# Performance work log

Hardware: AMD Instinct MI355X
Metric: run time of the kernel (lower is better)

## Reference

```python
import jax, jax.numpy as jnp
import numpy as np
import math

MUL = 16                      # num_in_features == num_out_features
LDIMS = (1, 3, 5)             # 0e, 1o, 2e  (lmax = 2)
FEAT = MUL * sum(LDIMS)       # 144 = irreps dim = number_of_basis
PATHS = [(0,0,0),(1,1,0),(2,2,0),
         (0,1,1),(1,0,1),(1,2,1),(2,1,1),
         (0,2,2),(1,1,2),(2,0,2),(2,2,2)]
DOT_PATHS = [(0,0,0),(1,1,0),(2,2,0)]

# ---------- real Wigner-3j / Clebsch-Gordan (e3nn convention), numpy precompute ----------

def _su2_cg(j1, m1, j2, m2, j3, m3):
    if m3 != m1 + m2:
        return 0.0
    f = math.factorial
    vmin = max(-j1 + j2 + m3, -j1 + m1, 0)
    vmax = min(j2 + j3 + m1, j3 - j1 + j2, j3 + m3)
    C = math.sqrt((2*j3+1) * f(j3+j1-j2) * f(j3-j1+j2) * f(j1+j2-j3)
                  * f(j3+m3) * f(j3-m3)
                  / (f(j1+j2+j3+1) * f(j1-m1) * f(j1+m1) * f(j2-m2) * f(j2+m2)))
    S = 0.0
    for v in range(vmin, vmax + 1):
        S += (-1.0)**(v + j2 + m2) * f(j2+j3+m1-v) * f(j1-m1+v) / (
            f(v) * f(j3-j1+j2-v) * f(j3+m3-v) * f(v+j1-j2-m3))
    return C * S

def _qmat(l):
    # complex -> real spherical-harmonic change of basis (e3nn convention)
    q = np.zeros((2*l+1, 2*l+1), dtype=np.complex128)
    for m in range(-l, 0):
        q[l+m, l+abs(m)] = 1.0/math.sqrt(2)
        q[l+m, l-abs(m)] = -1j/math.sqrt(2)
    q[l, l] = 1.0
    for m in range(1, l+1):
        q[l+m, l+abs(m)] = (-1)**m/math.sqrt(2)
        q[l+m, l-abs(m)] = 1j*(-1)**m/math.sqrt(2)
    return (-1j)**l * q

def _real_w3j(l1, l2, l3):
    C = np.zeros((2*l1+1, 2*l2+1, 2*l3+1))
    for i, m1 in enumerate(range(-l1, l1+1)):
        for j, m2 in enumerate(range(-l2, l2+1)):
            for k, m3 in enumerate(range(-l3, l3+1)):
                C[i, j, k] = _su2_cg(l1, m1, l2, m2, l3, m3)
    Cr = np.einsum('ij,kl,mn,ikn->jlm', _qmat(l1), _qmat(l2),
                   np.conj(_qmat(l3).T), C.astype(np.complex128))
    Cr = np.real(Cr)
    return (Cr / np.linalg.norm(Cr)).astype(np.float32)  # unit Frobenius norm (3j convention)

W3J = {p: _real_w3j(*p) for p in set(PATHS)}

# ---------- fully connected tensor product (component/element normalization) ----------

def _split(x):
    # blocked layout: [mul x 0e | mul x 1o | mul x 2e]
    n = x.shape[0]
    xs, o = [], 0
    for d in LDIMS:
        xs.append(x[:, o:o + MUL*d].reshape(n, MUL, d))
        o += MUL * d
    return xs

def _fctp(x1, x2, W):
    # W: [11, u, v, w] stacked per PATHS
    xs1, xs2 = _split(x1), _split(x2)
    n = x1.shape[0]
    n_paths = {l3: sum(1 for p in PATHS if p[2] == l3) for l3 in range(3)}
    outs = [None, None, None]
    for i, (l1, l2, l3) in enumerate(PATHS):
        C = jnp.asarray(W3J[(l1, l2, l3)])          # [i, j, k]
        scale = math.sqrt((2*l3 + 1) / (n_paths[l3] * MUL * MUL))
        a = jnp.einsum('nvj,ijk->nivk', xs2[l2], C)      # [n, i, v, k]
        b = jnp.einsum('nui,nivk->nuvk', xs1[l1], a)     # [n, u, v, k]
        o = scale * jnp.einsum('nuvk,uvw->nwk', b, W[i]) # [n, w, k]
        outs[l3] = o if outs[l3] is None else outs[l3] + o
    return jnp.concatenate([o.reshape(n, -1) for o in outs], axis=1)  # [n, 9*MUL]

def _dot(x1, x2, Wd):
    # FCTP(irreps_input, irreps_input, '0e'): paths (0,0,0),(1,1,0),(2,2,0), out mul = 1
    xs1, xs2 = _split(x1), _split(x2)
    fan = 3 * MUL * MUL
    acc = 0.0
    for i, (l1, l2, l3) in enumerate(DOT_PATHS):
        C = jnp.asarray(W3J[(l1, l2, l3)])[:, :, 0]      # [i, j]
        t = jnp.einsum('nui,ij,nvj->nuv', xs1[l1], C, xs2[l2])
        acc = acc + jnp.einsum('nuv,uv->n', t, Wd[i])
    return (acc * math.sqrt(1.0 / fan))[:, None]         # [n, 1]

def setup_inputs() -> dict:
    key = jax.random.key(0)
    ks = jax.random.split(key, 8)
    N = 50000
    return {
        'nodes_features': jax.random.normal(ks[0], (N, FEAT), jnp.float32),
        'degree_matrix': jax.random.normal(ks[1], (N,), jnp.float32),
        'edges_features_distance': jax.random.normal(ks[2], (N,), jnp.float32),
        'edges_features_bond': jax.random.normal(ks[3], (N,), jnp.float32),
        'w_q': jax.random.normal(ks[4], (11, MUL, MUL, MUL), jnp.float32),
        'w_k': jax.random.normal(ks[5], (11, MUL, MUL, MUL), jnp.float32),
        'w_v': jax.random.normal(ks[6], (11, MUL, MUL, MUL), jnp.float32),
        'w_dot': jax.random.normal(ks[7], (3, MUL, MUL), jnp.float32),
    }

def reference(nodes_features, degree_matrix, edges_features_distance,
              edges_features_bond, w_q, w_k, w_v, w_dot):
    # degree_matrix / edges_features_* are unused by the original forward
    x = nodes_features
    q = _fctp(x, x, w_q)                   # tp_q(x, x)
    k = _fctp(x, x, w_k)                   # tp_k(x, x)
    v = _fctp(x, x, w_v)                   # tp(x, x)
    d = _dot(q, k, w_dot)                  # [n, 1]
    e = jnp.exp(d / math.sqrt(float(FEAT)))
    attn = e / (e + 1e-10)                 # sum over last dim of size 1 + eps
    out = attn * v                         # dropout is identity in eval mode
    out = out.reshape(-1, MUL)             # view(-1, num_heads * num_out_features)
    return jax.nn.elu(out)                 # [9n, MUL]
```

## Files before the change

### kernel.cpp

```cpp
#include <hip/hip_runtime.h>
#include <math.h>

#define NP 11
#define NN 8

__device__ __constant__ int g_l1[NP]   = {0,1,2,0,1,1,2,0,1,2,2};
__device__ __constant__ int g_l2[NP]   = {0,1,2,1,0,2,1,2,1,0,2};
__device__ __constant__ int g_l3[NP]   = {0,0,0,1,1,1,1,2,2,2,2};
__device__ __constant__ int g_coff[NP] = {0,1,10,35,44,53,98,143,168,213,238};

typedef _Float16 half8 __attribute__((ext_vector_type(8)));
typedef _Float16 h2 __attribute__((ext_vector_type(2)));
typedef float f32x4 __attribute__((ext_vector_type(4)));

__device__ double dfact(int n){ double r=1.0; for(int i=2;i<=n;++i) r*=(double)i; return r; }

__device__ double su2_cg(int j1,int m1,int j2,int m2,int j3,int m3){
  if(m1+m2!=m3) return 0.0;
  int vmin=-j1+j2+m3; if(-j1+m1>vmin) vmin=-j1+m1; if(vmin<0) vmin=0;
  int vmax=j2+j3+m1; int t=j3-j1+j2; if(t<vmax) vmax=t; t=j3+m3; if(t<vmax) vmax=t;
  double C = sqrt((double)(2*j3+1)*dfact(j3+j1-j2)*dfact(j3-j1+j2)*dfact(j1+j2-j3)
      *dfact(j3+m3)*dfact(j3-m3)
      /(dfact(j1+j2+j3+1)*dfact(j1-m1)*dfact(j1+m1)*dfact(j2-m2)*dfact(j2+m2)));
  double S=0.0;
  for(int v=vmin;v<=vmax;++v){
    double sg = ((v+j2+m2)&1)? -1.0:1.0;
    S += sg*dfact(j2+j3+m1-v)*dfact(j1-m1+v)
        /(dfact(v)*dfact(j3-j1+j2-v)*dfact(j3+m3-v)*dfact(v+j1-j2-m3));
  }
  return C*S;
}

__device__ void qelem(int l,int r,int c,double &re,double &im){
  int m=r-l; double a=0.0,b=0.0; const double s=0.70710678118654752440;
  if(m<0){ if(c==l-m) a=s; else if(c==l+m) b=-s; }
  else if(m==0){ if(c==l) a=1.0; }
  else { double sg=(m&1)?-1.0:1.0; if(c==l+m) a=sg*s; else if(c==l-m) b=sg*s; }
  if(l==1){ double tt=a; a=b; b=-tt; }
  else if(l==2){ a=-a; b=-b; }
  re=a; im=b;
}

__global__ void w3j_init(float* __restrict__ ws){
  int p=blockIdx.x;
  int l1=g_l1[p], l2=g_l2[p], l3=g_l3[p];
  int d1=2*l1+1, d2=2*l2+1, d3=2*l3+1;
  int tot=d1*d2*d3;
  __shared__ double cg[125];
  __shared__ double outv[125];
  __shared__ double nrm;
  for(int t=threadIdx.x;t<tot;t+=blockDim.x){
    int i=t/(d2*d3), k=(t/d3)%d2, n=t%d3;
    cg[t]=su2_cg(l1,i-l1,l2,k-l2,l3,n-l3);
  }
  __syncthreads();
  for(int t=threadIdx.x;t<tot;t+=blockDim.x){
    int a=t/(d2*d3), b=(t/d3)%d2, c=t%d3;
    double sre=0.0;
    for(int i=0;i<d1;++i){ double q1r,q1i; qelem(l1,i,a,q1r,q1i);
      for(int k=0;k<d2;++k){ double q2r,q2i; qelem(l2,k,b,q2r,q2i);
        double pr=q1r*q2r-q1i*q2i, pi=q1r*q2i+q1i*q2r;
        for(int n=0;n<d3;++n){ double q3r,q3i; qelem(l3,n,c,q3r,q3i);
          sre += (pr*q3r + pi*q3i) * cg[(i*d2+k)*d3+n];
        }
      }
    }
    outv[t]=sre;
  }
  __syncthreads();
  if(threadIdx.x==0){
    double s=0.0; for(int t=0;t<tot;++t) s+=outv[t]*outv[t];
    nrm=sqrt(s);
  }
  __syncthreads();
  for(int t=threadIdx.x;t<tot;t+=blockDim.x)
    ws[g_coff[p]+t]=(float)(outv[t]/nrm);
}

__global__ void dtype_probe5(const unsigned short* p0,const unsigned short* p1,
                             const unsigned short* p2,const unsigned short* p3,
                             const unsigned short* p4,
                             int n0,int n1,int n2,int n3,int n4,
                             float* __restrict__ flags){
  __shared__ int cnt;
  const unsigned short* ps[5]={p0,p1,p2,p3,p4};
  int ns[5]={n0,n1,n2,n3,n4};
  int b=blockIdx.x;
  const unsigned short* p=ps[b]; int nelem=ns[b];
  if(threadIdx.x==0) cnt=0;
  __syncthreads();
  int M = nelem < 4096 ? nelem : 4096;
  int c=0;
  for(int t=threadIdx.x;t<M;t+=blockDim.x){
    unsigned e=((unsigned)p[t]>>7)&0xFFu;
    if(e!=0u && (e<0x70u || e>0x8Eu)) ++c;
  }
  atomicAdd(&cnt,c);
  __syncthreads();
  if(threadIdx.x==0) flags[b] = (cnt*8 > M) ? 1.0f : 0.0f;
}

__device__ __forceinline__ float bfu(unsigned int v){ return __uint_as_float(v<<16); }
__device__ __forceinline__ unsigned int rne16(float f){
  unsigned int ui=__float_as_uint(f);
  return (ui+0x7fffu+((ui>>16)&1u))>>16;
}
__device__ __forceinline__ unsigned short h16(float f){
  _Float16 h=(_Float16)f;
  return __builtin_bit_cast(unsigned short,h);
}

__global__ void w_prep(const unsigned short* __restrict__ wq,
                       const unsigned short* __restrict__ wk,
                       const unsigned short* __restrict__ wv,
                       const float* __restrict__ flags,
                       unsigned int* __restrict__ wpre){
  int p=blockIdx.x, tp=blockIdx.y;
  const unsigned short* ww=(tp==0)?wq:((tp==1)?wk:wv);
  int f32=flags[tp]!=0.0f;
  unsigned int* dst=wpre+(size_t)(p*3+tp)*2240;
  for(int t=threadIdx.x;t<2048;t+=256){
    int w=t>>7, uvp=t&127;
    float f0,f1;
    if(f32){
      const float* wf=(const float*)ww+(size_t)p*4096;
      f0=wf[(2*uvp)*16+w]; f1=wf[(2*uvp+1)*16+w];
    }else{
      const unsigned short* wsp=ww+(size_t)p*4096;
      f0=bfu(wsp[(2*uvp)*16+w]); f1=bfu(wsp[(2*uvp+1)*16+w]);
    }
    dst[w*140+uvp]=(unsigned int)h16(f0)|((unsigned int)h16(f1)<<16);
  }
}

template<int D1,int D2,int D3>
__device__ __forceinline__ void fusedAB(const float* __restrict__ sX,
                                        const float* __restrict__ cg, float scale,
                                        unsigned int* __restrict__ sAu,
                                        int wave, int lane, int nvalid){
  constexpr int O1=(D1==1)?0:((D1==3)?16:64);
  constexpr int O2=(D2==1)?0:((D2==3)?16:64);
  const int nn=lane>>3, vp=lane&7;
  if(nn>=nvalid) return;
  const float* xb=sX+nn*148;
  float x2a[D2],x2b[D2];
  #pragma unroll
  for(int j=0;j<D2;++j){
    x2a[j]=xb[O2+2*vp*D2+j]*scale;
    x2b[j]=xb[O2+(2*vp+1)*D2+j]*scale;
  }
  const int u0=wave*2;
  _Float16 x1a[D1],x1b[D1];
  #pragma unroll
  for(int i=0;i<D1;++i){
    x1a[i]=(_Float16)xb[O1+u0*D1+i];
    x1b[i]=(_Float16)xb[O1+(u0+1)*D1+i];
  }
  h2 acc0[D3],acc1[D3];
  #pragma unroll
  for(int k=0;k<D3;++k){ acc0[k]=(h2){(_Float16)0.f,(_Float16)0.f}; acc1[k]=acc0[k]; }
  #pragma unroll
  for(int i=0;i<D1;++i){
    h2 hva={x1a[i],x1a[i]}, hvb={x1b[i],x1b[i]};
    #pragma unroll
    for(int k=0;k<D3;++k){
      float fa=0.f,fb=0.f;
      #pragma unroll
      for(int j=0;j<D2;++j){
        float c=cg[(i*D2+j)*D3+k];
        fa+=c*x2a[j]; fb+=c*x2b[j];
      }
      h2 ar={(_Float16)fa,(_Float16)fb};
      acc0[k]+=hva*ar;
      acc1[k]+=hvb*ar;
    }
  }
  #pragma unroll
  for(int k=0;k<D3;++k){
    sAu[(k*8+nn)*140+u0*8+vp]    =__builtin_bit_cast(unsigned int,acc0[k]);
    sAu[(k*8+nn)*140+(u0+1)*8+vp]=__builtin_bit_cast(unsigned int,acc1[k]);
  }
}

template<int L3>
__device__ __forceinline__ void stage2_acc(const unsigned int* __restrict__ sAu,
                                           const unsigned int* __restrict__ wp_path,
                                           f32x4& a0, f32x4& a1,
                                           int n16, int quad, int wave){
  constexpr int P=(L3+1)*3;
  if(wave<P){
    int tp=wave%3, Mt=wave/3;
    const unsigned int* ap=sAu+(Mt*16+n16)*140+quad*4;
    const uint4* bp=(const uint4*)(wp_path+tp*2240+n16*140+quad*4);
    uint4 b[8];
    #pragma unroll
    for(int ks=0;ks<8;++ks) b[ks]=bp[ks*4];
    f32x4 a=a0;
    #pragma unroll
    for(int ks=0;ks<8;++ks)
      a=__builtin_amdgcn_mfma_f32_16x16x32_f16(
          *reinterpret_cast<const half8*>(ap+ks*16),
          __builtin_bit_cast(half8,b[ks]),a,0,0,0);
    a0=a;
  }
  if(L3==2 && wave==0){
    const unsigned int* ap=sAu+(2*16+n16)*140+quad*4;
    const uint4* bp=(const uint4*)(wp_path+2*2240+n16*140+quad*4);
    uint4 b[8];
    #pragma unroll
    for(int ks=0;ks<8;++ks) b[ks]=bp[ks*4];
    f32x4 a=a1;
    #pragma unroll
    for(int ks=0;ks<8;++ks)
      a=__builtin_amdgcn_mfma_f32_16x16x32_f16(
          *reinterpret_cast<const half8*>(ap+ks*16),
          __builtin_bit_cast(half8,b[ks]),a,0,0,0);
    a1=a;
  }
}

template<int L3>
__device__ __forceinline__ void stage2_out(const f32x4& a0, const f32x4& a1,
                                           float* __restrict__ sO,
                                           int n16, int quad, int wave){
  constexpr int D3=2*L3+1;
  constexpr int OO=(L3==0)?0:((L3==1)?16:64);
  constexpr int P=(L3+1)*3;
  if(wave<P){
    int tp=wave%3, Mt=wave/3;
    #pragma unroll
    for(int reg=0;reg<4;++reg){
      int row=Mt*16+quad*4+reg;
      int k=row>>3, node=row&7;
      if(k<D3) sO[node*440+tp*144+OO+n16*D3+k]=a0[reg];
    }
  }
  if(L3==2 && wave==0){
    #pragma unroll
    for(int reg=0;reg<4;++reg){
      int row=32+quad*4+reg;
      int k=row>>3, node=row&7;
      if(k<D3) sO[node*440+2*144+OO+n16*D3+k]=a1[reg];
    }
  }
}

__global__ __launch_bounds__(512,6) void tfn_main(
    const unsigned short* __restrict__ xin,
    const unsigned int* __restrict__ wpre,
    const unsigned short* __restrict__ wd,
    const float* __restrict__ c3j,
    unsigned short* __restrict__ outp, int N)
{
  __shared__ __align__(16) unsigned int sAu[48*140];
  __shared__ float sO[NN*440];
  __shared__ float sX[NN*148];
  __shared__ float sWd[768];

  const int tid=threadIdx.x;
  const int wave=tid>>6, lane=tid&63;
  const int n16=lane&15, quad=lane>>4;
  const int node0=blockIdx.x*NN;
  const int nvalid=(N-node0)<NN?(N-node0):NN;

  const int xf32 = c3j[363]!=0.0f;
  const int df32 = c3j[367]!=0.0f;

  if(!xf32){
    for(int t=tid;t<NN*36;t+=512){
      int nn=t/36, w4=t%36;
      if(nn<nvalid){
        uint2 u=((const uint2*)(xin+(size_t)(node0+nn)*144))[w4];
        float* dst=&sX[nn*148+w4*4];
        dst[0]=bfu(u.x&0xffffu); dst[1]=bfu(u.x>>16);
        dst[2]=bfu(u.y&0xffffu); dst[3]=bfu(u.y>>16);
      }
    }
  }else{
    const float* xf=(const float*)xin;
    for(int t=tid;t<NN*144;t+=512){
      int nn=t/144, f=t%144;
      if(nn<nvalid) sX[nn*148+f]=xf[(size_t)(node0+nn)*144+f];
    }
  }
  if(!df32){ for(int t=tid;t<768;t+=512) sWd[t]=bfu((unsigned int)wd[t]); }
  else     { const float* wdf=(const float*)wd; for(int t=tid;t<768;t+=512) sWd[t]=wdf[t]; }
  __syncthreads();

  const float scl[3]={0.03608439182435161f,0.05412658773652741f,0.06987712429686843f};

  #define PATH_STEP(P_,D1_,D2_,D3_) { \
    fusedAB<D1_,D2_,D3_>(sX,c3j+g_coff[P_],scl[(D3_-1)/2],sAu,wave,lane,nvalid); \
    __syncthreads(); \
    stage2_acc<(D3_-1)/2>(sAu,wpre+(size_t)P_*6720,a0,a1,n16,quad,wave); \
    __syncthreads(); }

  {
    f32x4 a0={0.f,0.f,0.f,0.f}, a1={0.f,0.f,0.f,0.f};
    PATH_STEP(0,1,1,1)
    PATH_STEP(1,3,3,1)
    PATH_STEP(2,5,5,1)
    stage2_out<0>(a0,a1,sO,n16,quad,wave);
  }
  {
    f32x4 a0={0.f,0.f,0.f,0.f}, a1={0.f,0.f,0.f,0.f};
    PATH_STEP(3,1,3,3)
    PATH_STEP(4,3,1,3)
    PATH_STEP(5,3,5,3)
    PATH_STEP(6,5,3,3)
    stage2_out<1>(a0,a1,sO,n16,quad,wave);
  }
  {
    f32x4 a0={0.f,0.f,0.f,0.f}, a1={0.f,0.f,0.f,0.f};
    PATH_STEP(7,1,5,5)
    PATH_STEP(8,3,3,5)
    PATH_STEP(9,5,1,5)
    PATH_STEP(10,5,5,5)
    stage2_out<2>(a0,a1,sO,n16,quad,wave);
  }
  #undef PATH_STEP
  __syncthreads();

  {
    int node=wave;
    if(node<nvalid){
      const float c0=c3j[0], c1=c3j[1], c2=c3j[10];
      const float* qv=sO+node*440;
      const float* kv=qv+144;
      const int v=lane&15, ug=lane>>4;
      float k0=kv[v];
      float k1[3],k2[5];
      #pragma unroll
      for(int j=0;j<3;++j) k1[j]=kv[16+v*3+j];
      #pragma unroll
      for(int m=0;m<5;++m) k2[m]=kv[64+v*5+m];
      float part=0.f;
      #pragma unroll
      for(int t=0;t<4;++t){
        int u=ug+4*t;
        float d0=qv[u]*k0;
        float d1=0.f;
        #pragma unroll
        for(int j=0;j<3;++j) d1+=qv[16+u*3+j]*k1[j];
        float d2=0.f;
        #pragma unroll
        for(int m=0;m<5;++m) d2+=qv[64+u*5+m]*k2[m];
        part+=sWd[u*16+v]*(c0*d0)+sWd[256+u*16+v]*(c1*d1)+sWd[512+u*16+v]*(c2*d2);
      }
      #pragma unroll
      for(int off=1;off<64;off<<=1) part+=__shfl_xor(part,off,64);
      float dd=part*0.03608439182435161f;
      float ex=dd*(1.0f/12.0f);
      ex=fminf(fmaxf(ex,-80.f),80.f);
      float e=expf(ex);
      float attn=e/(e+1e-10f);
      const float* vv=sO+node*440+288;
      if(!xf32){
        unsigned short* ob=outp+(size_t)(node0+node)*144;
        for(int f=lane;f<144;f+=64){
          float val=attn*vv[f];
          float r=(val>0.f)?val:expm1f(val);
          ob[f]=(unsigned short)rne16(r);
        }
      }else{
        float* ob=(float*)outp+(size_t)(node0+node)*144;
        for(int f=lane;f<144;f+=64){
          float val=attn*vv[f];
          ob[f]=(val>0.f)?val:expm1f(val);
        }
      }
    }
  }
}

extern "C" void kernel_launch(void* const* d_in, const int* in_sizes, int n_in,
                              void* d_out, int out_size, void* d_ws, size_t ws_size,
                              hipStream_t stream){
  (void)n_in; (void)out_size; (void)ws_size;
  const unsigned short* x =(const unsigned short*)d_in[0];
  const unsigned short* wq=(const unsigned short*)d_in[4];
  const unsigned short* wk=(const unsigned short*)d_in[5];
  const unsigned short* wv=(const unsigned short*)d_in[6];
  const unsigned short* wd=(const unsigned short*)d_in[7];
  float* c3j=(float*)d_ws;
  unsigned int* wpre=(unsigned int*)((float*)d_ws+512);
  int N=in_sizes[0]/144;
  w3j_init<<<dim3(NP),dim3(128),0,stream>>>(c3j);
  dtype_probe5<<<dim3(5),dim3(256),0,stream>>>(x,wq,wk,wv,wd,
      in_sizes[0],in_sizes[4],in_sizes[5],in_sizes[6],in_sizes[7],c3j+363);
  w_prep<<<dim3(NP,3),dim3(256),0,stream>>>(wq,wk,wv,c3j+364,wpre);
  int nb=(N+NN-1)/NN;
  tfn_main<<<dim3(nb),dim3(512),0,stream>>>(x,wpre,wd,c3j,(unsigned short*)d_out,N);
}
```

Baseline: 393.1 us.

## Pack CG coefficients and node features as half2 for packed fp16 contraction

```diff
diff --git a/kernel.cpp b/kernel.cpp
--- a/kernel.cpp
+++ b/kernel.cpp
@@ -110,6 +110,18 @@
   return __builtin_bit_cast(unsigned short,h);
 }
 
+__global__ void c_pack(const float* __restrict__ c3j, unsigned int* __restrict__ cgh){
+  int p=blockIdx.x;
+  int d1=2*g_l1[p]+1, d2=2*g_l2[p]+1, d3=2*g_l3[p]+1;
+  const float scl_[3]={0.03608439182435161f,0.05412658773652741f,0.06987712429686843f};
+  float s=scl_[g_l3[p]];
+  int tot=d1*d2*d3;
+  for(int t=threadIdx.x;t<tot;t+=64){
+    unsigned int h=(unsigned int)h16(c3j[g_coff[p]+t]*s);
+    cgh[g_coff[p]+t]=h|(h<<16);
+  }
+}
+
 __global__ void w_prep(const unsigned short* __restrict__ wq,
                        const unsigned short* __restrict__ wk,
                        const unsigned short* __restrict__ wv,
@@ -120,65 +132,61 @@
   int f32=flags[tp]!=0.0f;
   unsigned int* dst=wpre+(size_t)(p*3+tp)*2240;
   for(int t=threadIdx.x;t<2048;t+=256){
-    int w=t>>7, uvp=t&127;
+    int w=t>>7, c=t&127, u=c&15, vp=c>>4;
+    int i0=(u*16+2*vp)*16+w, i1=i0+16;
     float f0,f1;
     if(f32){
       const float* wf=(const float*)ww+(size_t)p*4096;
-      f0=wf[(2*uvp)*16+w]; f1=wf[(2*uvp+1)*16+w];
+      f0=wf[i0]; f1=wf[i1];
     }else{
       const unsigned short* wsp=ww+(size_t)p*4096;
-      f0=bfu(wsp[(2*uvp)*16+w]); f1=bfu(wsp[(2*uvp+1)*16+w]);
-    }
-    dst[w*140+uvp]=(unsigned int)h16(f0)|((unsigned int)h16(f1)<<16);
+      f0=bfu(wsp[i0]); f1=bfu(wsp[i1]);
+    }
+    dst[w*140+c]=(unsigned int)h16(f0)|((unsigned int)h16(f1)<<16);
   }
 }
 
 template<int D1,int D2,int D3>
-__device__ __forceinline__ void fusedAB(const float* __restrict__ sX,
-                                        const float* __restrict__ cg, float scale,
+__device__ __forceinline__ void fusedAB(const unsigned int* __restrict__ sXp,
+                                        const unsigned int* __restrict__ sXd,
+                                        const unsigned int* __restrict__ cgp,
                                         unsigned int* __restrict__ sAu,
                                         int wave, int lane, int nvalid){
   constexpr int O1=(D1==1)?0:((D1==3)?16:64);
-  constexpr int O2=(D2==1)?0:((D2==3)?16:64);
+  constexpr int O2P=(D2==1)?0:((D2==3)?8:32);
   const int nn=lane>>3, vp=lane&7;
   if(nn>=nvalid) return;
-  const float* xb=sX+nn*148;
-  float x2a[D2],x2b[D2];
+  h2 x2p[D2];
   #pragma unroll
-  for(int j=0;j<D2;++j){
-    x2a[j]=xb[O2+2*vp*D2+j]*scale;
-    x2b[j]=xb[O2+(2*vp+1)*D2+j]*scale;
-  }
+  for(int j=0;j<D2;++j) x2p[j]=__builtin_bit_cast(h2,sXp[nn*76+O2P+vp*D2+j]);
   const int u0=wave*2;
-  _Float16 x1a[D1],x1b[D1];
+  h2 x1a[D1],x1b[D1];
   #pragma unroll
   for(int i=0;i<D1;++i){
-    x1a[i]=(_Float16)xb[O1+u0*D1+i];
-    x1b[i]=(_Float16)xb[O1+(u0+1)*D1+i];
+    x1a[i]=__builtin_bit_cast(h2,sXd[nn*148+O1+u0*D1+i]);
+    x1b[i]=__builtin_bit_cast(h2,sXd[nn*148+O1+(u0+1)*D1+i]);
   }
   h2 acc0[D3],acc1[D3];
   #pragma unroll
   for(int k=0;k<D3;++k){ acc0[k]=(h2){(_Float16)0.f,(_Float16)0.f}; acc1[k]=acc0[k]; }
   #pragma unroll
   for(int i=0;i<D1;++i){
-    h2 hva={x1a[i],x1a[i]}, hvb={x1b[i],x1b[i]};
     #pragma unroll
     for(int k=0;k<D3;++k){
-      float fa=0.f,fb=0.f;
+      h2 ar=(h2){(_Float16)0.f,(_Float16)0.f};
       #pragma unroll
-      for(int j=0;j<D2;++j){
-        float c=cg[(i*D2+j)*D3+k];
-        fa+=c*x2a[j]; fb+=c*x2b[j];
-      }
-      h2 ar={(_Float16)fa,(_Float16)fb};
-      acc0[k]+=hva*ar;
-      acc1[k]+=hvb*ar;
+      for(int j=0;j<D2;++j)
+        ar+=__builtin_bit_cast(h2,cgp[(i*D2+j)*D3+k])*x2p[j];
+      acc0[k]+=x1a[i]*ar;
+      acc1[k]+=x1b[i]*ar;
     }
   }
   #pragma unroll
   for(int k=0;k<D3;++k){
-    sAu[(k*8+nn)*140+u0*8+vp]    =__builtin_bit_cast(unsigned int,acc0[k]);
-    sAu[(k*8+nn)*140+(u0+1)*8+vp]=__builtin_bit_cast(unsigned int,acc1[k]);
+    uint2 st;
+    st.x=__builtin_bit_cast(unsigned int,acc0[k]);
+    st.y=__builtin_bit_cast(unsigned int,acc1[k]);
+    *(uint2*)(sAu+(k*8+nn)*140+vp*16+u0)=st;
   }
 }
 
@@ -248,13 +256,15 @@
 __global__ __launch_bounds__(512,6) void tfn_main(
     const unsigned short* __restrict__ xin,
     const unsigned int* __restrict__ wpre,
+    const unsigned int* __restrict__ cgh,
     const unsigned short* __restrict__ wd,
     const float* __restrict__ c3j,
     unsigned short* __restrict__ outp, int N)
 {
   __shared__ __align__(16) unsigned int sAu[48*140];
   __shared__ float sO[NN*440];
-  __shared__ float sX[NN*148];
+  __shared__ __align__(8) unsigned int sXp[NN*76];
+  __shared__ __align__(8) unsigned int sXd[NN*148];
   __shared__ float sWd[768];
 
   const int tid=threadIdx.x;
@@ -266,12 +276,13 @@
   const int xf32 = c3j[363]!=0.0f;
   const int df32 = c3j[367]!=0.0f;
 
+  float* scratch=sO;
   if(!xf32){
     for(int t=tid;t<NN*36;t+=512){
       int nn=t/36, w4=t%36;
       if(nn<nvalid){
         uint2 u=((const uint2*)(xin+(size_t)(node0+nn)*144))[w4];
-        float* dst=&sX[nn*148+w4*4];
+        float* dst=&scratch[nn*144+w4*4];
         dst[0]=bfu(u.x&0xffffu); dst[1]=bfu(u.x>>16);
         dst[2]=bfu(u.y&0xffffu); dst[3]=bfu(u.y>>16);
       }
@@ -280,17 +291,30 @@
     const float* xf=(const float*)xin;
     for(int t=tid;t<NN*144;t+=512){
       int nn=t/144, f=t%144;
-      if(nn<nvalid) sX[nn*148+f]=xf[(size_t)(node0+nn)*144+f];
+      if(nn<nvalid) scratch[nn*144+f]=xf[(size_t)(node0+nn)*144+f];
     }
   }
   if(!df32){ for(int t=tid;t<768;t+=512) sWd[t]=bfu((unsigned int)wd[t]); }
   else     { const float* wdf=(const float*)wd; for(int t=tid;t<768;t+=512) sWd[t]=wdf[t]; }
   __syncthreads();
 
-  const float scl[3]={0.03608439182435161f,0.05412658773652741f,0.06987712429686843f};
+  for(int t=tid;t<NN*144;t+=512){
+    int nn=t/144, f=t-nn*144;
+    unsigned int h=(unsigned int)h16(scratch[t]);
+    sXd[nn*148+f]=h|(h<<16);
+  }
+  for(int t=tid;t<NN*72;t+=512){
+    int nn=t/72, g=t-nn*72;
+    int fa,fb;
+    if(g<8){ fa=2*g; fb=fa+1; }
+    else if(g<32){ int gg=g-8; int vp=gg/3, j=gg-3*vp; fa=16+(2*vp)*3+j; fb=fa+3; }
+    else { int gg=g-32; int vp=gg/5, j=gg-5*vp; fa=64+(2*vp)*5+j; fb=fa+5; }
+    sXp[nn*76+g]=(unsigned int)h16(scratch[nn*144+fa])|((unsigned int)h16(scratch[nn*144+fb])<<16);
+  }
+  __syncthreads();
 
   #define PATH_STEP(P_,D1_,D2_,D3_) { \
-    fusedAB<D1_,D2_,D3_>(sX,c3j+g_coff[P_],scl[(D3_-1)/2],sAu,wave,lane,nvalid); \
+    fusedAB<D1_,D2_,D3_>(sXp,sXd,cgh+g_coff[P_],sAu,wave,lane,nvalid); \
     __syncthreads(); \
     stage2_acc<(D3_-1)/2>(sAu,wpre+(size_t)P_*6720,a0,a1,n16,quad,wave); \
     __syncthreads(); }
@@ -383,12 +407,14 @@
   const unsigned short* wv=(const unsigned short*)d_in[6];
   const unsigned short* wd=(const unsigned short*)d_in[7];
   float* c3j=(float*)d_ws;
-  unsigned int* wpre=(unsigned int*)((float*)d_ws+512);
+  unsigned int* cgh=(unsigned int*)d_ws+1024;
+  unsigned int* wpre=(unsigned int*)d_ws+2048;
   int N=in_sizes[0]/144;
   w3j_init<<<dim3(NP),dim3(128),0,stream>>>(c3j);
   dtype_probe5<<<dim3(5),dim3(256),0,stream>>>(x,wq,wk,wv,wd,
       in_sizes[0],in_sizes[4],in_sizes[5],in_sizes[6],in_sizes[7],c3j+363);
+  c_pack<<<dim3(NP),dim3(64),0,stream>>>(c3j,cgh);
   w_prep<<<dim3(NP,3),dim3(256),0,stream>>>(wq,wk,wv,c3j+364,wpre);
   int nb=(N+NN-1)/NN;
-  tfn_main<<<dim3(nb),dim3(512),0,stream>>>(x,wpre,wd,c3j,(unsigned short*)d_out,N);
-}
+  tfn_main<<<dim3(nb),dim3(512),0,stream>>>(x,wpre,cgh,wd,c3j,(unsigned short*)d_out,N);
+}
```

After: 385.2 us. -2.0%, faster.
